# Optimization experiments

Measured on AMD Instinct MI355X. Metric: run time of the kernel, lower is better.

## Reference

```python
import jax, jax.numpy as jnp
import numpy as np

S, E, H = 4096, 1024, 16
D = E // H
N_SEG = 64


def setup_inputs() -> dict:
    key = jax.random.key(0)
    ks = jax.random.split(key, 11)
    scale = 0.02
    inp = {
        "x": jax.random.normal(ks[0], (S, E), dtype=jnp.float32),
        "Wq": jax.random.normal(ks[1], (E, E), dtype=jnp.float32) * scale,
        "bq": jax.random.normal(ks[2], (E,), dtype=jnp.float32) * scale,
        "Wk": jax.random.normal(ks[3], (E, E), dtype=jnp.float32) * scale,
        "bk": jax.random.normal(ks[4], (E,), dtype=jnp.float32) * scale,
        "Wv": jax.random.normal(ks[5], (E, E), dtype=jnp.float32) * scale,
        "bv": jax.random.normal(ks[6], (E,), dtype=jnp.float32) * scale,
        "Wo": jax.random.normal(ks[7], (E, E), dtype=jnp.float32) * scale,
        "bo": jax.random.normal(ks[8], (E,), dtype=jnp.float32) * scale,
        "segment_ids": jnp.sort(jax.random.randint(ks[9], (S,), 0, N_SEG)).astype(jnp.int32),
        "pos": 100,
    }
    return inp


def reference(x, Wq, bq, Wk, bk, Wv, bv, Wo, bo, segment_ids, pos):
    # torch Linear: y = x @ W.T + b
    q = (x @ Wq.T + bq).reshape(S, H, D)  # [S, H, D]
    k = (x @ Wk.T + bk).reshape(S, H, D)
    v = (x @ Wv.T + bv).reshape(S, H, D)

    # same-segment mask (contiguous segments from gene-structure dividers)
    mask = segment_ids[:, None] == segment_ids[None, :]  # [S, S]

    # NOTE: original leaves out-of-segment scores at 0 (not -inf) and applies
    # softmax over the FULL row; also no 1/sqrt(d) scaling. Reproduce exactly.
    scores = jnp.einsum("shd,thd->hst", q, k)            # [H, S, S]
    scores = jnp.where(mask[None, :, :], scores, 0.0)
    weights = jax.nn.softmax(scores, axis=-1)            # softmax over full row

    wv = jnp.einsum("hst,thd->shd", weights, v).reshape(S, E)
    out = wv @ Wo.T + bo                                  # [S, E]

    # mean over the main context: tokens sharing pos's segment
    main = (segment_ids == segment_ids[pos]).astype(out.dtype)  # [S]
    result = (out * main[:, None]).sum(axis=0) / main.sum()
    return result
```

## Files before the change

### kernel.cpp

```cpp
#include <hip/hip_runtime.h>
#include <math.h>

#define SS 4096
#define EE 1024
#define HH 16
#define DD 64
#define RMAX 128
#define NCOL 128
#define NTR  8
#define NRED 8
#define NPROJ 384
#define NREDB 96
#define NBG 64
#define NVS 16
#define NATT 256

#define OFF_SUMX  64
#define OFF_BGA   1088
#define OFF_BETA  2112
#define OFF_ALPHA 3136
#define OFF_VSUM  3200
#define OFF_PART  8192
#define OFF_XT    (OFF_PART + EE * NCOL)
#define OFF_QH    (OFF_XT + EE * RMAX)
#define OFF_KTH   (OFF_QH + HH * RMAX * DD)
#define OFF_VH    (OFF_KTH + HH * DD * RMAX)
#define OFF_YP    (OFF_VH + HH * RMAX * DD)

__device__ __forceinline__ void seg_scan(const int* __restrict__ seg,
                                         const int* __restrict__ posp,
                                         int* sh, int& s0, int& L) {
    if (threadIdx.x == 0) { sh[0] = SS; sh[1] = -1; }
    __syncthreads();
    int sid = seg[posp[0]];
    int lmin = SS, lmax = -1;
    for (int i = threadIdx.x; i < SS; i += 256)
        if (seg[i] == sid) { lmin = min(lmin, i); lmax = max(lmax, i); }
#pragma unroll
    for (int off = 32; off; off >>= 1) {
        lmin = min(lmin, __shfl_xor(lmin, off));
        lmax = max(lmax, __shfl_xor(lmax, off));
    }
    if ((threadIdx.x & 63) == 0) { atomicMin(&sh[0], lmin); atomicMax(&sh[1], lmax); }
    __syncthreads();
    s0 = sh[0];
    L  = sh[1] - sh[0] + 1;
    if (L > RMAX) L = RMAX;
    if (L < 1)    L = 1;
}

__global__ __launch_bounds__(256) void d0_kernel(
    const float* __restrict__ x, const int* __restrict__ seg,
    const int* __restrict__ posp, float* __restrict__ ws) {
    int bid = blockIdx.x, tid = threadIdx.x;
    if (bid < NCOL) {
        float* partT = ws + OFF_PART;
        int r0 = bid * (SS / NCOL);
        const float4* x4 = (const float4*)x;
        float4 a = make_float4(0.f, 0.f, 0.f, 0.f);
#pragma unroll 8
        for (int r = 0; r < SS / NCOL; ++r) {
            float4 v = x4[(size_t)(r0 + r) * 256 + tid];
            a.x += v.x; a.y += v.y; a.z += v.z; a.w += v.w;
        }
        partT[(size_t)(4 * tid + 0) * NCOL + bid] = a.x;
        partT[(size_t)(4 * tid + 1) * NCOL + bid] = a.y;
        partT[(size_t)(4 * tid + 2) * NCOL + bid] = a.z;
        partT[(size_t)(4 * tid + 3) * NCOL + bid] = a.w;
        return;
    }
    __shared__ float t[128 * 129];
    __shared__ int sh[2];
    int s0, L;
    seg_scan(seg, posp, sh, s0, L);
    int kb = bid - NCOL;
    if (kb == 0 && tid == 0) { ((int*)ws)[0] = s0; ((int*)ws)[1] = L; }
    int k0 = kb * 128;
    float* xT = ws + OFF_XT;
    for (int idx = tid; idx < 128 * 32; idx += 256) {
        int r = idx >> 5, c4 = idx & 31;
        float4 v = make_float4(0.f, 0.f, 0.f, 0.f);
        if (r < L) v = *(const float4*)(x + (size_t)(s0 + r) * EE + k0 + c4 * 4);
        t[r * 129 + c4 * 4 + 0] = v.x;
        t[r * 129 + c4 * 4 + 1] = v.y;
        t[r * 129 + c4 * 4 + 2] = v.z;
        t[r * 129 + c4 * 4 + 3] = v.w;
    }
    __syncthreads();
    for (int idx = tid; idx < 128 * 32; idx += 256) {
        int k = idx >> 5, r4 = idx & 31;
        float4 o;
        o.x = t[(r4 * 4 + 0) * 129 + k];
        o.y = t[(r4 * 4 + 1) * 129 + k];
        o.z = t[(r4 * 4 + 2) * 129 + k];
        o.w = t[(r4 * 4 + 3) * 129 + k];
        *(float4*)(xT + (size_t)(k0 + k) * RMAX + r4 * 4) = o;
    }
}

__global__ __launch_bounds__(256) void d1_kernel(
    const float* __restrict__ Wq, const float* __restrict__ Wk,
    const float* __restrict__ Wv, float* __restrict__ ws) {
    int bid = blockIdx.x, tid = threadIdx.x;
    if (bid < NRED) {
        if (bid == 0) {
            for (int i = tid; i < 1088; i += 256) (ws + OFF_BETA)[i] = 0.f;
        }
        const float* partT = ws + OFF_PART;
        int e  = bid * 128 + (tid >> 1);
        int c0 = (tid & 1) * 64;
        const float4* p4 = (const float4*)(partT + (size_t)e * NCOL + c0);
        float4 s4 = make_float4(0.f, 0.f, 0.f, 0.f);
#pragma unroll
        for (int i = 0; i < 16; ++i) {
            float4 v = p4[i];
            s4.x += v.x; s4.y += v.y; s4.z += v.z; s4.w += v.w;
        }
        float s = s4.x + s4.y + s4.z + s4.w;
        s += __shfl_xor(s, 1);
        if ((tid & 1) == 0) (ws + OFF_SUMX)[e] = s;
        return;
    }
    __shared__ float wsL[32 * 256];
    int L  = ((const int*)ws)[1];
    int Lp = (L + 63) & ~63;
    int nh = Lp >> 6;
    int pid = bid - NRED;
    int kc  = pid & 3;
    int et  = (pid >> 2) & 31;
    int m   = pid >> 7;
    const float* W = (m == 0) ? Wq : ((m == 1) ? Wk : Wv);
    int k0 = kc * 256;

    {
#pragma unroll
        for (int i = 0; i < 8; ++i) {
            int idx = tid + i * 256;
            int e = idx >> 6, k4 = idx & 63;
            float4 v = *(const float4*)(W + (size_t)(et * 32 + e) * EE + k0 + k4 * 4);
            *(float4*)&wsL[e * 256 + k4 * 4] = v;
        }
    }
    __syncthreads();

    int lane = tid & 63;
    int w4   = tid >> 6;
    int e0w  = w4 * 8;
    const float* x0 = ws + OFF_XT + lane;
    float acc[2][8];
#pragma unroll
    for (int hh = 0; hh < 2; ++hh)
#pragma unroll
        for (int j = 0; j < 8; ++j) acc[hh][j] = 0.f;
    for (int kk = 0; kk < 256; kk += 8) {
        float xv0[8], xv1[8];
#pragma unroll
        for (int u = 0; u < 8; ++u)
            xv0[u] = x0[(size_t)(k0 + kk + u) * RMAX];
        if (nh == 2) {
#pragma unroll
            for (int u = 0; u < 8; ++u)
                xv1[u] = x0[(size_t)(k0 + kk + u) * RMAX + 64];
        }
#pragma unroll
        for (int j = 0; j < 8; ++j) {
            const float4* wp = (const float4*)&wsL[(e0w + j) * 256 + kk];
            float4 wa = wp[0], wb = wp[1];
            acc[0][j] += wa.x * xv0[0] + wa.y * xv0[1] + wa.z * xv0[2] + wa.w * xv0[3]
                       + wb.x * xv0[4] + wb.y * xv0[5] + wb.z * xv0[6] + wb.w * xv0[7];
            if (nh == 2)
                acc[1][j] += wa.x * xv1[0] + wa.y * xv1[1] + wa.z * xv1[2] + wa.w * xv1[3]
                           + wb.x * xv1[4] + wb.y * xv1[5] + wb.z * xv1[6] + wb.w * xv1[7];
        }
    }
    float* yp = ws + OFF_YP + ((size_t)(kc * 3 + m) * EE) * RMAX;
#pragma unroll
    for (int j = 0; j < 8; ++j) {
        int e = et * 32 + e0w + j;
        yp[(size_t)e * RMAX + lane] = acc[0][j];
        if (nh == 2) yp[(size_t)e * RMAX + 64 + lane] = acc[1][j];
    }
}

__global__ __launch_bounds__(256) void d1b_kernel(
    const float* __restrict__ bq, const float* __restrict__ bk,
    const float* __restrict__ bv, float* __restrict__ ws) {
    int bid = blockIdx.x, tid = threadIdx.x;
    int L = ((const int*)ws)[1];
    int m  = bid / 32;
    int et = bid % 32;
    const float* b = (m == 0) ? bq : ((m == 1) ? bk : bv);
    float* qh  = ws + OFF_QH;
    float* kTh = ws + OFF_KTH;
    float* vh  = ws + OFF_VH;
    const float* yp = ws + OFF_YP;
    int r4 = (tid & 31) * 4;
    int ee = tid >> 5;
#pragma unroll
    for (int ep = 0; ep < 4; ++ep) {
        int e = et * 32 + ep * 8 + ee;
        size_t base = (size_t)e * RMAX + r4;
        float4 s = make_float4(0.f, 0.f, 0.f, 0.f);
#pragma unroll
        for (int kc = 0; kc < 4; ++kc) {
            float4 v = *(const float4*)(yp + ((size_t)(kc * 3 + m) * EE) * RMAX + base);
            s.x += v.x; s.y += v.y; s.z += v.z; s.w += v.w;
        }
        float bb = b[e];
        float o[4] = {s.x + bb, s.y + bb, s.z + bb, s.w + bb};
#pragma unroll
        for (int i = 0; i < 4; ++i) if (r4 + i >= L) o[i] = 0.f;
        int h = e >> 6, d = e & 63;
        if (m == 1) {
            *(float4*)(kTh + (size_t)(h * DD + d) * RMAX + r4) =
                make_float4(o[0], o[1], o[2], o[3]);
        } else {
            float* y = (m == 0) ? qh : vh;
#pragma unroll
            for (int i = 0; i < 4; ++i)
                y[((size_t)h * RMAX + r4 + i) * DD + d] = o[i];
        }
    }
}

__global__ __launch_bounds__(256) void d2_kernel(
    const float* __restrict__ Wv, const float* __restrict__ bv,
    float* __restrict__ ws) {
    __shared__ float qS[4 * 64];
    __shared__ float wS[4 * 128];
    __shared__ float vp_[4][64];
    const float* sumx = ws + OFF_SUMX;
    float* bgA    = ws + OFF_BGA;
    float* betap  = ws + OFF_BETA;
    float* alphap = ws + OFF_ALPHA;
    float* vsumh  = ws + OFF_VSUM;
    const float* qh  = ws + OFF_QH;
    const float* kTh = ws + OFF_KTH;
    const float* vh  = ws + OFF_VH;

    int bid = blockIdx.x, tid = threadIdx.x;
    int lane = tid & 63, wave = tid >> 6;
    int L  = ((const int*)ws)[1];
    int Lp = (L + 63) & ~63;

    if (bid < NBG) {
        int e = bid * 16 + (tid >> 4);
        int j = tid & 15;
        const float4* wr  = (const float4*)(Wv + (size_t)e * EE);
        const float4* sx4 = (const float4*)sumx;
        float p = 0.f;
#pragma unroll
        for (int jj = 0; jj < 16; ++jj) {
            float4 w = wr[jj * 16 + j], z = sx4[jj * 16 + j];
            p += w.x * z.x + w.y * z.y + w.z * z.z + w.w * z.w;
        }
        p += __shfl_xor(p, 8);
        p += __shfl_xor(p, 4);
        p += __shfl_xor(p, 2);
        p += __shfl_xor(p, 1);
        if (j == 0) bgA[e] = p + (float)SS * bv[e];
        return;
    }
    if (bid < NBG + NVS) {
        int h = bid - NBG;
        float s = 0.f;
        for (int t = wave; t < Lp; t += 4)
            s += vh[((size_t)h * RMAX + t) * DD + lane];
        vp_[wave][lane] = s;
        __syncthreads();
        if (wave == 0)
            vsumh[h * DD + lane] = vp_[0][lane] + vp_[1][lane]
                                 + vp_[2][lane] + vp_[3][lane];
        return;
    }

    int aid = bid - NBG - NVS;
    int gidbase = aid * 4 + wave;
    int pairs = L * HH;
    float* qSw = qS + wave * 64;
    float* wSw = wS + wave * 128;
    for (int wg = gidbase; wg < pairs; wg += NATT * 4) {
        int h = wg & (HH - 1);
        int r = wg >> 4;
        qSw[lane] = qh[((size_t)h * RMAX + r) * DD + lane];
        float s0 = 0.f, s1 = 0.f;
#pragma unroll
        for (int d = 0; d < 64; ++d) {
            float qd = qSw[d];
            const float* kr = kTh + (size_t)(h * DD + d) * RMAX;
            s0 += qd * kr[lane];
            s1 += qd * kr[64 + lane];
        }
        float v0 = (lane < L)      ? s0 : -3.0e38f;
        float v1 = (64 + lane < L) ? s1 : -3.0e38f;
        float m = fmaxf(0.f, fmaxf(v0, v1));
#pragma unroll
        for (int off = 32; off; off >>= 1) m = fmaxf(m, __shfl_xor(m, off));
        float w0 = (lane < L)      ? __expf(s0 - m) : 0.f;
        float w1 = (64 + lane < L) ? __expf(s1 - m) : 0.f;
        float Zl = w0 + w1;
#pragma unroll
        for (int off = 32; off; off >>= 1) Zl += __shfl_xor(Zl, off);
        float em = __expf(-m);
        float Z  = Zl + (float)(SS - L) * em;
        wSw[lane]      = w0;
        wSw[64 + lane] = w1;
        float acc = 0.f;
#pragma unroll 16
        for (int t = 0; t < Lp; ++t)
            acc += wSw[t] * vh[((size_t)h * RMAX + t) * DD + lane];
        float invZ = 1.0f / Z;
        atomicAdd(&betap[h * DD + lane], acc * invZ);
        if (lane == 0) atomicAdd(&alphap[h], em * invZ);
    }
}

__global__ __launch_bounds__(256) void d3_kernel(
    const float* __restrict__ Wo, const float* __restrict__ bo,
    const float* __restrict__ ws, float* __restrict__ out) {
    __shared__ float z[EE];
    int tid = threadIdx.x;
    int lane = tid & 63, wave = tid >> 6;
    int L = ((const int*)ws)[1];

    {
        int h = tid >> 4;
        float4 beta = ((const float4*)(ws + OFF_BETA))[tid];
        float  a    = (ws + OFF_ALPHA)[h];
        float4 g    = ((const float4*)(ws + OFF_BGA))[tid];
        float4 vs   = ((const float4*)(ws + OFF_VSUM))[tid];
        ((float4*)z)[tid] = make_float4(beta.x + a * (g.x - vs.x),
                                        beta.y + a * (g.y - vs.y),
                                        beta.z + a * (g.z - vs.z),
                                        beta.w + a * (g.w - vs.w));
    }
    __syncthreads();

    int e = blockIdx.x * 4 + wave;
    const float4* wr = (const float4*)(Wo + (size_t)e * EE);
    const float4* z4 = (const float4*)z;
    float p = 0.f;
#pragma unroll
    for (int it = 0; it < 4; ++it) {
        float4 w = wr[it * 64 + lane], zz = z4[it * 64 + lane];
        p += w.x * zz.x + w.y * zz.y + w.z * zz.z + w.w * zz.w;
    }
#pragma unroll
    for (int off = 32; off; off >>= 1) p += __shfl_xor(p, off);
    if (lane == 0) out[e] = bo[e] + p / (float)L;
}

extern "C" void kernel_launch(void* const* d_in, const int* in_sizes, int n_in,
                              void* d_out, int out_size, void* d_ws, size_t ws_size,
                              hipStream_t stream) {
    const float* x   = (const float*)d_in[0];
    const float* Wq  = (const float*)d_in[1];
    const float* bq  = (const float*)d_in[2];
    const float* Wk  = (const float*)d_in[3];
    const float* bk  = (const float*)d_in[4];
    const float* Wv  = (const float*)d_in[5];
    const float* bv  = (const float*)d_in[6];
    const float* Wo  = (const float*)d_in[7];
    const float* bo  = (const float*)d_in[8];
    const int*   seg = (const int*)d_in[9];
    const int*   pos = (const int*)d_in[10];
    float*       out = (float*)d_out;
    float*       ws  = (float*)d_ws;

    d0_kernel<<<NCOL + NTR, 256, 0, stream>>>(x, seg, pos, ws);
    d1_kernel<<<NRED + NPROJ, 256, 0, stream>>>(Wq, Wk, Wv, ws);
    d1b_kernel<<<NREDB, 256, 0, stream>>>(bq, bk, bv, ws);
    d2_kernel<<<NBG + NVS + NATT, 256, 0, stream>>>(Wv, bv, ws);
    d3_kernel<<<EE / 4, 256, 0, stream>>>(Wo, bo, ws, out);
}
```

Measured before the change: 80.20 us.

## Retile QKV projection into more blocks with transposed weight tile and prefetched x

Doubles the number of projection blocks (16 output features per block instead of 32) and stores the weight tile transposed in padded shared memory, so each warp reads four features per float4. The x loads are double-buffered in registers, and each warp starts at a staggered k offset to spread memory traffic. The nh==2 branch is removed, so both 64-row halves are always computed, which costs extra work when the segment length is small. The aim is more parallelism and better latency hiding in the small-M GEMM.

Result: faster. 71.12 us (-11.3%).

```diff
diff --git a/kernel.cpp b/kernel.cpp
--- a/kernel.cpp
+++ b/kernel.cpp
@@ -9,7 +9,7 @@
 #define NCOL 128
 #define NTR  8
 #define NRED 8
-#define NPROJ 384
+#define NPROJ 768
 #define NREDB 96
 #define NBG 64
 #define NVS 16
@@ -121,65 +121,88 @@
         if ((tid & 1) == 0) (ws + OFF_SUMX)[e] = s;
         return;
     }
-    __shared__ float wsL[32 * 256];
-    int L  = ((const int*)ws)[1];
-    int Lp = (L + 63) & ~63;
-    int nh = Lp >> 6;
+    __shared__ float ws2[256 * 20];
     int pid = bid - NRED;
     int kc  = pid & 3;
-    int et  = (pid >> 2) & 31;
-    int m   = pid >> 7;
+    int rem = pid >> 2;
+    int m   = rem / 64;
+    int eb  = rem - m * 64;
     const float* W = (m == 0) ? Wq : ((m == 1) ? Wk : Wv);
-    int k0 = kc * 256;
+    int kq = kc * 256;
+    int e0t = eb * 16;
 
     {
 #pragma unroll
-        for (int i = 0; i < 8; ++i) {
-            int idx = tid + i * 256;
+        for (int p = 0; p < 4; ++p) {
+            int idx = tid + p * 256;
             int e = idx >> 6, k4 = idx & 63;
-            float4 v = *(const float4*)(W + (size_t)(et * 32 + e) * EE + k0 + k4 * 4);
-            *(float4*)&wsL[e * 256 + k4 * 4] = v;
+            float4 v = *(const float4*)(W + (size_t)(e0t + e) * EE + kq + k4 * 4);
+            ws2[(k4 * 4 + 0) * 20 + e] = v.x;
+            ws2[(k4 * 4 + 1) * 20 + e] = v.y;
+            ws2[(k4 * 4 + 2) * 20 + e] = v.z;
+            ws2[(k4 * 4 + 3) * 20 + e] = v.w;
         }
     }
     __syncthreads();
 
     int lane = tid & 63;
-    int w4   = tid >> 6;
-    int e0w  = w4 * 8;
-    const float* x0 = ws + OFF_XT + lane;
-    float acc[2][8];
-#pragma unroll
-    for (int hh = 0; hh < 2; ++hh)
-#pragma unroll
-        for (int j = 0; j < 8; ++j) acc[hh][j] = 0.f;
-    for (int kk = 0; kk < 256; kk += 8) {
-        float xv0[8], xv1[8];
-#pragma unroll
-        for (int u = 0; u < 8; ++u)
-            xv0[u] = x0[(size_t)(k0 + kk + u) * RMAX];
-        if (nh == 2) {
-#pragma unroll
-            for (int u = 0; u < 8; ++u)
-                xv1[u] = x0[(size_t)(k0 + kk + u) * RMAX + 64];
-        }
-#pragma unroll
-        for (int j = 0; j < 8; ++j) {
-            const float4* wp = (const float4*)&wsL[(e0w + j) * 256 + kk];
-            float4 wa = wp[0], wb = wp[1];
-            acc[0][j] += wa.x * xv0[0] + wa.y * xv0[1] + wa.z * xv0[2] + wa.w * xv0[3]
-                       + wb.x * xv0[4] + wb.y * xv0[5] + wb.z * xv0[6] + wb.w * xv0[7];
-            if (nh == 2)
-                acc[1][j] += wa.x * xv1[0] + wa.y * xv1[1] + wa.z * xv1[2] + wa.w * xv1[3]
-                           + wb.x * xv1[4] + wb.y * xv1[5] + wb.z * xv1[6] + wb.w * xv1[7];
+    int w4 = __builtin_amdgcn_readfirstlane(tid >> 6);
+    int eo = w4 * 4;
+    int ko = (eb & 31) * 8;
+    const float* xA = ws + OFF_XT + lane;
+    const float* xB = ws + OFF_XT + 64 + lane;
+    float accA0 = 0.f, accA1 = 0.f, accA2 = 0.f, accA3 = 0.f;
+    float accB0 = 0.f, accB1 = 0.f, accB2 = 0.f, accB3 = 0.f;
+    float xa0[8], xb0[8], xa1[8], xb1[8];
+#pragma unroll
+    for (int u = 0; u < 8; ++u) {
+        int k = kq + ((ko + u) & 255);
+        xa0[u] = xA[(size_t)k * RMAX];
+        xb0[u] = xB[(size_t)k * RMAX];
+    }
+    for (int kk = 0; kk < 256; kk += 16) {
+        int g1 = ko + kk + 8, g2 = ko + kk + 16;
+#pragma unroll
+        for (int u = 0; u < 8; ++u) {
+            int k = kq + ((g1 + u) & 255);
+            xa1[u] = xA[(size_t)k * RMAX];
+            xb1[u] = xB[(size_t)k * RMAX];
+        }
+#pragma unroll
+        for (int u = 0; u < 8; ++u) {
+            int kl = (ko + kk + u) & 255;
+            float4 w = *(const float4*)&ws2[kl * 20 + eo];
+            accA0 += w.x * xa0[u]; accA1 += w.y * xa0[u];
+            accA2 += w.z * xa0[u]; accA3 += w.w * xa0[u];
+            accB0 += w.x * xb0[u]; accB1 += w.y * xb0[u];
+            accB2 += w.z * xb0[u]; accB3 += w.w * xb0[u];
+        }
+#pragma unroll
+        for (int u = 0; u < 8; ++u) {
+            int k = kq + ((g2 + u) & 255);
+            xa0[u] = xA[(size_t)k * RMAX];
+            xb0[u] = xB[(size_t)k * RMAX];
+        }
+#pragma unroll
+        for (int u = 0; u < 8; ++u) {
+            int kl = (g1 + u) & 255;
+            float4 w = *(const float4*)&ws2[kl * 20 + eo];
+            accA0 += w.x * xa1[u]; accA1 += w.y * xa1[u];
+            accA2 += w.z * xa1[u]; accA3 += w.w * xa1[u];
+            accB0 += w.x * xb1[u]; accB1 += w.y * xb1[u];
+            accB2 += w.z * xb1[u]; accB3 += w.w * xb1[u];
         }
     }
     float* yp = ws + OFF_YP + ((size_t)(kc * 3 + m) * EE) * RMAX;
-#pragma unroll
-    for (int j = 0; j < 8; ++j) {
-        int e = et * 32 + e0w + j;
-        yp[(size_t)e * RMAX + lane] = acc[0][j];
-        if (nh == 2) yp[(size_t)e * RMAX + 64 + lane] = acc[1][j];
-    }
+    int e0 = e0t + eo;
+    yp[(size_t)(e0 + 0) * RMAX + lane] = accA0;
+    yp[(size_t)(e0 + 1) * RMAX + lane] = accA1;
+    yp[(size_t)(e0 + 2) * RMAX + lane] = accA2;
+    yp[(size_t)(e0 + 3) * RMAX + lane] = accA3;
+    yp[(size_t)(e0 + 0) * RMAX + 64 + lane] = accB0;
+    yp[(size_t)(e0 + 1) * RMAX + 64 + lane] = accB1;
+    yp[(size_t)(e0 + 2) * RMAX + 64 + lane] = accB2;
+    yp[(size_t)(e0 + 3) * RMAX + 64 + lane] = accB3;
 }
 
 __global__ __launch_bounds__(256) void d1b_kernel(
```
